# Kernel tuning notes

Measured on AMD Instinct MI355X. Metric: run time of the kernel, lower is better.

## Reference

```python
import jax, jax.numpy as jnp
import numpy as np

N_NODES = 50000
N_EDGES = 600000
IN_FEATS = 128
HIDDEN = 256
OUT_FEATS = 64


def setup_inputs() -> dict:
    key = jax.random.key(0)
    ks = jax.random.split(key, 12)
    inv = lambda n: 1.0 / np.sqrt(n)
    return {
        "x": jax.random.normal(ks[0], (N_NODES, IN_FEATS), dtype=jnp.float32),
        "edge_index": jax.random.randint(ks[1], (2, N_EDGES), 0, N_NODES, dtype=jnp.int64),
        "W_sage": jax.random.normal(ks[2], (IN_FEATS, IN_FEATS), dtype=jnp.float32) * inv(IN_FEATS),
        "W1a": jax.random.normal(ks[3], (IN_FEATS, HIDDEN), dtype=jnp.float32) * inv(IN_FEATS),
        "b1a": jax.random.normal(ks[4], (HIDDEN,), dtype=jnp.float32) * 0.01,
        "W1b": jax.random.normal(ks[5], (HIDDEN, OUT_FEATS), dtype=jnp.float32) * inv(HIDDEN),
        "b1b": jax.random.normal(ks[6], (OUT_FEATS,), dtype=jnp.float32) * 0.01,
        "W2a": jax.random.normal(ks[7], (IN_FEATS, HIDDEN), dtype=jnp.float32) * inv(IN_FEATS),
        "b2a": jax.random.normal(ks[8], (HIDDEN,), dtype=jnp.float32) * 0.01,
        "W2b": jax.random.normal(ks[9], (HIDDEN, OUT_FEATS), dtype=jnp.float32) * inv(HIDDEN),
        "b2b": jax.random.normal(ks[10], (OUT_FEATS,), dtype=jnp.float32) * 0.01,
    }


def reference(x, edge_index, W_sage, W1a, b1a, W1b, b1b, W2a, b2a, W2b, b2b):
    n = x.shape[0]
    src, dst = edge_index[0], edge_index[1]
    # SAGEConv mean aggregation: mean over incoming neighbor (source) features at each target node
    summed = jax.ops.segment_sum(x[src], dst, num_segments=n)          # [N, in]
    deg = jax.ops.segment_sum(jnp.ones_like(src, dtype=x.dtype), dst, num_segments=n)
    mean = summed / jnp.maximum(deg, 1.0)[:, None]                     # nodes w/o neighbors -> 0
    x_1hop = mean @ W_sage                                             # lin_l, no root, no bias
    # dual MLP branches (dropout is identity in eval mode)
    out1 = jax.nn.relu(x @ W1a + b1a) @ W1b + b1b
    out2 = jax.nn.relu(x_1hop @ W2a + b2a) @ W2b + b2b
    return out1 + out2
```

## Files before the change

### kernel.cpp

```cpp
#include <hip/hip_runtime.h>

#define N_NODES 50000
#define N_PAD   50048
#define N_EDGES 600000
#define IN_F 128
#define HID 256
#define OUT_F 64
#define ROWS 16
#define SLOTS 56
#define NBLK (N_PAD / ROWS)
#define EPT 4

typedef __attribute__((ext_vector_type(8))) short bf16x8;
typedef __attribute__((ext_vector_type(4))) float f32x4;

__device__ inline short f2bf(float f) {
    unsigned u = __builtin_bit_cast(unsigned, f);
    u += 0x7fffu + ((u >> 16) & 1u);
    return (short)(u >> 16);
}
__device__ inline float bflo(unsigned u) { return __builtin_bit_cast(float, u << 16); }
__device__ inline float bfhi(unsigned u) { return __builtin_bit_cast(float, u & 0xffff0000u); }

__global__ __launch_bounds__(256) void build_kernel(
    const int* __restrict__ ei, int* __restrict__ cursor,
    unsigned short* __restrict__ esrc)
{
    int t0 = blockIdx.x * (256 * EPT) + threadIdx.x;
    int src[EPT], dst[EPT], p[EPT];
    bool v[EPT];
    #pragma unroll
    for (int i = 0; i < EPT; ++i) {
        int e = t0 + i * 256;
        v[i] = e < N_EDGES;
        int ee = v[i] ? e : 0;
        src[i] = ei[ee];
        dst[i] = ei[N_EDGES + ee];
    }
    #pragma unroll
    for (int i = 0; i < EPT; ++i)
        p[i] = v[i] ? atomicAdd(&cursor[dst[i]], 1) : SLOTS;
    #pragma unroll
    for (int i = 0; i < EPT; ++i)
        if (v[i] && p[i] < SLOTS)
            esrc[(size_t)dst[i] * SLOTS + p[i]] = (unsigned short)src[i];
}

__global__ __launch_bounds__(256) void prep_kernel(
    const float* __restrict__ x, short* __restrict__ xb,
    const float* __restrict__ Wsg, const float* __restrict__ W2a,
    const float* __restrict__ W1a, const float* __restrict__ W1b,
    const float* __restrict__ W2b,
    short* __restrict__ F1a, short* __restrict__ F1b,
    short* __restrict__ Fc,  short* __restrict__ F2b)
{
    const int bid = blockIdx.x, t = threadIdx.x;
    if (bid < 3125) {
        int i = bid * 256 + t;
        float4 a0 = *reinterpret_cast<const float4*>(x + (size_t)i * 8);
        float4 a1 = *reinterpret_cast<const float4*>(x + (size_t)i * 8 + 4);
        bf16x8 v;
        v[0] = f2bf(a0.x); v[1] = f2bf(a0.y); v[2] = f2bf(a0.z); v[3] = f2bf(a0.w);
        v[4] = f2bf(a1.x); v[5] = f2bf(a1.y); v[6] = f2bf(a1.z); v[7] = f2bf(a1.w);
        *reinterpret_cast<bf16x8*>(xb + (size_t)i * 8) = v;
        return;
    }
    int cid = (bid - 3125) * 256 + t;
    if (cid >= 6144 && cid < 10240) {
        int c = cid - 6144;
        int lane = c & 63, rem = c >> 6;
        int ks = rem & 3, nt = rem >> 2;
        int col = nt * 16 + (lane & 15);
        int k0 = ks * 32 + (lane >> 4) * 8;
        float acc[8] = {0.f, 0.f, 0.f, 0.f, 0.f, 0.f, 0.f, 0.f};
        for (int m0 = 0; m0 < 128; m0 += 8) {
            float wcol[8];
            #pragma unroll
            for (int mm = 0; mm < 8; ++mm)
                wcol[mm] = W2a[(size_t)(m0 + mm) * HID + col];
            #pragma unroll
            for (int j = 0; j < 8; ++j) {
                #pragma unroll
                for (int mm = 0; mm < 8; ++mm)
                    acc[j] = fmaf(Wsg[(size_t)(k0 + j) * IN_F + m0 + mm], wcol[mm], acc[j]);
            }
        }
        bf16x8 v;
        #pragma unroll
        for (int j = 0; j < 8; ++j) v[j] = f2bf(acc[j]);
        *reinterpret_cast<bf16x8*>(Fc + (size_t)c * 8) = v;
    } else {
        const float* src; short* dst; int N, KST, base;
        if      (cid < 4096)  { src = W1a; dst = F1a; N = 256; KST = 4; base = 0; }
        else if (cid < 6144)  { src = W1b; dst = F1b; N = 64;  KST = 8; base = 4096; }
        else                  { src = W2b; dst = F2b; N = 64;  KST = 8; base = 10240; }
        int c = cid - base;
        int lane = c & 63;
        int rem = c >> 6;
        int ks = rem % KST;
        int nt = rem / KST;
        int col = nt * 16 + (lane & 15);
        int k0 = ks * 32 + (lane >> 4) * 8;
        bf16x8 v;
        #pragma unroll
        for (int j = 0; j < 8; ++j)
            v[j] = f2bf(src[(size_t)(k0 + j) * N + col]);
        *reinterpret_cast<bf16x8*>(dst + (size_t)c * 8) = v;
    }
}

__device__ inline bf16x8 afrag_lds128(const short* S, int lane, int ks) {
    int row = lane & 15, g = lane >> 4;
    int chunk = (ks * 4 + g) ^ row;
    return *reinterpret_cast<const bf16x8*>(
        reinterpret_cast<const char*>(S) + row * 256 + chunk * 16);
}
__device__ inline bf16x8 afrag_lds256(const short* S, int lane, int ks) {
    int row = lane & 15, g = lane >> 4;
    int chunk = (ks * 4 + g) ^ row;
    return *reinterpret_cast<const bf16x8*>(
        reinterpret_cast<const char*>(S) + row * 512 + chunk * 16);
}

__device__ inline void stage1_relu(const bf16x8 afr[4], short* Hs,
                                   const short* __restrict__ Waf,
                                   const float* __restrict__ ba,
                                   int w, int lane)
{
    const int row16 = lane & 15, g = lane >> 4;
    #pragma unroll
    for (int i = 0; i < 4; ++i) {
        int nt = w * 4 + i;
        f32x4 acc = {0.f, 0.f, 0.f, 0.f};
        __builtin_amdgcn_s_setprio(1);
        #pragma unroll
        for (int ks = 0; ks < 4; ++ks) {
            bf16x8 b = *reinterpret_cast<const bf16x8*>(
                Waf + ((size_t)(nt * 4 + ks) * 64 + lane) * 8);
            acc = __builtin_amdgcn_mfma_f32_16x16x32_bf16(afr[ks], b, acc, 0, 0, 0);
        }
        __builtin_amdgcn_s_setprio(0);
        int col = nt * 16 + row16;
        float bias = ba[col];
        #pragma unroll
        for (int reg = 0; reg < 4; ++reg) {
            int hrow = g * 4 + reg;
            float v = fmaxf(acc[reg] + bias, 0.0f);
            *reinterpret_cast<short*>(reinterpret_cast<char*>(Hs)
                + hrow * 512 + ((((col >> 3) ^ hrow) & 31) * 16) + (col & 7) * 2) = f2bf(v);
        }
    }
}

__device__ inline f32x4 stage2_acc(const short* Hs, const short* __restrict__ Wbf,
                                   int w, int lane, f32x4 acc)
{
    __builtin_amdgcn_s_setprio(1);
    #pragma unroll
    for (int ks = 0; ks < 8; ++ks) {
        bf16x8 a = afrag_lds256(Hs, lane, ks);
        bf16x8 b = *reinterpret_cast<const bf16x8*>(
            Wbf + ((size_t)(w * 8 + ks) * 64 + lane) * 8);
        acc = __builtin_amdgcn_mfma_f32_16x16x32_bf16(a, b, acc, 0, 0, 0);
    }
    __builtin_amdgcn_s_setprio(0);
    return acc;
}

__global__ __launch_bounds__(256) void fused_kernel(
    const short* __restrict__ xb, const unsigned short* __restrict__ esrc,
    const int* __restrict__ deg,
    const short* __restrict__ F1a, const float* __restrict__ b1a,
    const short* __restrict__ F1b, const float* __restrict__ b1b,
    const short* __restrict__ Fc,  const float* __restrict__ b2a,
    const short* __restrict__ F2b, const float* __restrict__ b2b,
    float* __restrict__ out)
{
    __shared__ short Ms[16 * 128];
    __shared__ short Hs[16 * 256];
    const int t = threadIdx.x, w = t >> 6, lane = t & 63;
    const long r0 = (long)blockIdx.x * ROWS;
    const int row16 = lane & 15, g = lane >> 4;

    #pragma unroll
    for (int nn = 0; nn < 4; ++nn) {
        int row = w * 4 + nn;
        long node = r0 + row;
        int d = deg[node]; d = min(d, SLOTS);
        int slot = min(lane, SLOTS - 1);
        int my = esrc[(size_t)node * SLOTS + slot];
        float ax = 0.f, ay = 0.f;
        for (int j = 0; j < d; j += 16) {
            unsigned u[16];
            #pragma unroll
            for (int k = 0; k < 16; ++k) {
                int cidx = min(j + k, d - 1);
                int s = __builtin_amdgcn_readlane(my, cidx);
                u[k] = *reinterpret_cast<const unsigned*>(xb + (size_t)s * IN_F + lane * 2);
            }
            #pragma unroll
            for (int k = 0; k < 16; ++k) {
                float wk = (j + k < d) ? 1.0f : 0.0f;
                ax = fmaf(bflo(u[k]), wk, ax);
                ay = fmaf(bfhi(u[k]), wk, ay);
            }
        }
        float inv = (d > 0) ? 1.0f / (float)d : 0.0f;
        ax *= inv; ay *= inv;
        int chunk = (lane >> 2) ^ row;
        unsigned packed = (unsigned)(unsigned short)f2bf(ax)
                        | ((unsigned)(unsigned short)f2bf(ay) << 16);
        *reinterpret_cast<unsigned*>(reinterpret_cast<char*>(Ms)
            + row * 256 + chunk * 16 + (lane & 3) * 4) = packed;
    }
    __syncthreads();

    {
        bf16x8 afr[4];
        #pragma unroll
        for (int ks = 0; ks < 4; ++ks) afr[ks] = afrag_lds128(Ms, lane, ks);
        stage1_relu(afr, Hs, Fc, b2a, w, lane);
    }
    __syncthreads();

    f32x4 oacc = {0.f, 0.f, 0.f, 0.f};
    oacc = stage2_acc(Hs, F2b, w, lane, oacc);
    __syncthreads();

    {
        bf16x8 afr[4];
        const short* xrow = xb + (size_t)(r0 + row16) * IN_F + g * 8;
        #pragma unroll
        for (int ks = 0; ks < 4; ++ks)
            afr[ks] = *reinterpret_cast<const bf16x8*>(xrow + ks * 32);
        stage1_relu(afr, Hs, F1a, b1a, w, lane);
    }
    __syncthreads();

    oacc = stage2_acc(Hs, F1b, w, lane, oacc);
    {
        int col = w * 16 + row16;
        float bias = b1b[col] + b2b[col];
        #pragma unroll
        for (int reg = 0; reg < 4; ++reg) {
            long row = r0 + g * 4 + reg;
            if (row < N_NODES)
                out[row * OUT_F + col] = oacc[reg] + bias;
        }
    }
}

extern "C" void kernel_launch(void* const* d_in, const int* in_sizes, int n_in,
                              void* d_out, int out_size, void* d_ws, size_t ws_size,
                              hipStream_t stream)
{
    const float* x   = (const float*)d_in[0];
    const int*   ei  = (const int*)d_in[1];
    const float* Wsg = (const float*)d_in[2];
    const float* W1a = (const float*)d_in[3];
    const float* b1a = (const float*)d_in[4];
    const float* W1b = (const float*)d_in[5];
    const float* b1b = (const float*)d_in[6];
    const float* W2a = (const float*)d_in[7];
    const float* b2a = (const float*)d_in[8];
    const float* W2b = (const float*)d_in[9];
    const float* b2b = (const float*)d_in[10];
    float* out = (float*)d_out;

    int* cursor = (int*)d_ws;
    unsigned short* esrc = (unsigned short*)(cursor + N_PAD);
    short* F1a = (short*)(esrc + (size_t)N_PAD * SLOTS);
    short* F1b = F1a + 4096 * 8;
    short* Fc  = F1b + 2048 * 8;
    short* F2b = Fc + 4096 * 8;
    short* xb  = F2b + 2048 * 8;

    hipMemsetAsync(cursor, 0, N_PAD * sizeof(int), stream);
    build_kernel<<<(N_EDGES + 256 * EPT - 1) / (256 * EPT), 256, 0, stream>>>(
        ei, cursor, esrc);
    prep_kernel<<<3173, 256, 0, stream>>>(x, xb, Wsg, W2a, W1a, W1b, W2b,
                                          F1a, F1b, Fc, F2b);
    fused_kernel<<<NBLK, 256, 0, stream>>>(xb, esrc, cursor,
                                           F1a, b1a, F1b, b1b,
                                           Fc, b2a, F2b, b2b, out);
}
```

Baseline: 122.0 us.

## Merge memset into prep, interleave dual MLP branches, pad gather with zero row

Drops the separate hipMemsetAsync and zeroes the cursor inside the prep kernel, which also writes a zero row after xb. Build now runs after prep with one edge per thread. In the fused kernel, the gather uses a wave-uniform degree and sends out-of-range slots to the zero row, so the masked FMAs become plain adds. The two MLP branches are computed together with separate LDS buffers, which removes two barriers and interleaves independent MFMA chains. The cost is more shared memory per block and extra register pressure.

```diff
diff --git a/kernel.cpp b/kernel.cpp
--- a/kernel.cpp
+++ b/kernel.cpp
@@ -9,7 +9,7 @@
 #define ROWS 16
 #define SLOTS 56
 #define NBLK (N_PAD / ROWS)
-#define EPT 4
+#define ZERO_ROW N_NODES
 
 typedef __attribute__((ext_vector_type(8))) short bf16x8;
 typedef __attribute__((ext_vector_type(4))) float f32x4;
@@ -21,30 +21,6 @@
 }
 __device__ inline float bflo(unsigned u) { return __builtin_bit_cast(float, u << 16); }
 __device__ inline float bfhi(unsigned u) { return __builtin_bit_cast(float, u & 0xffff0000u); }
-
-__global__ __launch_bounds__(256) void build_kernel(
-    const int* __restrict__ ei, int* __restrict__ cursor,
-    unsigned short* __restrict__ esrc)
-{
-    int t0 = blockIdx.x * (256 * EPT) + threadIdx.x;
-    int src[EPT], dst[EPT], p[EPT];
-    bool v[EPT];
-    #pragma unroll
-    for (int i = 0; i < EPT; ++i) {
-        int e = t0 + i * 256;
-        v[i] = e < N_EDGES;
-        int ee = v[i] ? e : 0;
-        src[i] = ei[ee];
-        dst[i] = ei[N_EDGES + ee];
-    }
-    #pragma unroll
-    for (int i = 0; i < EPT; ++i)
-        p[i] = v[i] ? atomicAdd(&cursor[dst[i]], 1) : SLOTS;
-    #pragma unroll
-    for (int i = 0; i < EPT; ++i)
-        if (v[i] && p[i] < SLOTS)
-            esrc[(size_t)dst[i] * SLOTS + p[i]] = (unsigned short)src[i];
-}
 
 __global__ __launch_bounds__(256) void prep_kernel(
     const float* __restrict__ x, short* __restrict__ xb,
@@ -52,7 +28,8 @@
     const float* __restrict__ W1a, const float* __restrict__ W1b,
     const float* __restrict__ W2b,
     short* __restrict__ F1a, short* __restrict__ F1b,
-    short* __restrict__ Fc,  short* __restrict__ F2b)
+    short* __restrict__ Fc,  short* __restrict__ F2b,
+    int* __restrict__ cursor)
 {
     const int bid = blockIdx.x, t = threadIdx.x;
     if (bid < 3125) {
@@ -63,6 +40,17 @@
         v[0] = f2bf(a0.x); v[1] = f2bf(a0.y); v[2] = f2bf(a0.z); v[3] = f2bf(a0.w);
         v[4] = f2bf(a1.x); v[5] = f2bf(a1.y); v[6] = f2bf(a1.z); v[7] = f2bf(a1.w);
         *reinterpret_cast<bf16x8*>(xb + (size_t)i * 8) = v;
+        return;
+    }
+    if (bid >= 3200) {
+        int i = (bid - 3200) * 256 + t;
+        bf16x8 z = {0, 0, 0, 0, 0, 0, 0, 0};
+        *reinterpret_cast<bf16x8*>(xb + (size_t)N_NODES * IN_F + (size_t)i * 8) = z;
+        return;
+    }
+    if (bid >= 3173) {
+        for (int i = (bid - 3173) * 256 + t; i < N_PAD; i += 27 * 256)
+            cursor[i] = 0;
         return;
     }
     int cid = (bid - 3125) * 256 + t;
@@ -109,6 +97,18 @@
     }
 }
 
+__global__ __launch_bounds__(256) void build_kernel(
+    const int* __restrict__ ei, int* __restrict__ cursor,
+    unsigned short* __restrict__ esrc)
+{
+    int e = blockIdx.x * 256 + threadIdx.x;
+    if (e >= N_EDGES) return;
+    int src = ei[e];
+    int dst = ei[N_EDGES + e];
+    int p = atomicAdd(&cursor[dst], 1);
+    if (p < SLOTS) esrc[(size_t)dst * SLOTS + p] = (unsigned short)src;
+}
+
 __device__ inline bf16x8 afrag_lds128(const short* S, int lane, int ks) {
     int row = lane & 15, g = lane >> 4;
     int chunk = (ks * 4 + g) ^ row;
@@ -120,51 +120,6 @@
     int chunk = (ks * 4 + g) ^ row;
     return *reinterpret_cast<const bf16x8*>(
         reinterpret_cast<const char*>(S) + row * 512 + chunk * 16);
-}
-
-__device__ inline void stage1_relu(const bf16x8 afr[4], short* Hs,
-                                   const short* __restrict__ Waf,
-                                   const float* __restrict__ ba,
-                                   int w, int lane)
-{
-    const int row16 = lane & 15, g = lane >> 4;
-    #pragma unroll
-    for (int i = 0; i < 4; ++i) {
-        int nt = w * 4 + i;
-        f32x4 acc = {0.f, 0.f, 0.f, 0.f};
-        __builtin_amdgcn_s_setprio(1);
-        #pragma unroll
-        for (int ks = 0; ks < 4; ++ks) {
-            bf16x8 b = *reinterpret_cast<const bf16x8*>(
-                Waf + ((size_t)(nt * 4 + ks) * 64 + lane) * 8);
-            acc = __builtin_amdgcn_mfma_f32_16x16x32_bf16(afr[ks], b, acc, 0, 0, 0);
-        }
-        __builtin_amdgcn_s_setprio(0);
-        int col = nt * 16 + row16;
-        float bias = ba[col];
-        #pragma unroll
-        for (int reg = 0; reg < 4; ++reg) {
-            int hrow = g * 4 + reg;
-            float v = fmaxf(acc[reg] + bias, 0.0f);
-            *reinterpret_cast<short*>(reinterpret_cast<char*>(Hs)
-                + hrow * 512 + ((((col >> 3) ^ hrow) & 31) * 16) + (col & 7) * 2) = f2bf(v);
-        }
-    }
-}
-
-__device__ inline f32x4 stage2_acc(const short* Hs, const short* __restrict__ Wbf,
-                                   int w, int lane, f32x4 acc)
-{
-    __builtin_amdgcn_s_setprio(1);
-    #pragma unroll
-    for (int ks = 0; ks < 8; ++ks) {
-        bf16x8 a = afrag_lds256(Hs, lane, ks);
-        bf16x8 b = *reinterpret_cast<const bf16x8*>(
-            Wbf + ((size_t)(w * 8 + ks) * 64 + lane) * 8);
-        acc = __builtin_amdgcn_mfma_f32_16x16x32_bf16(a, b, acc, 0, 0, 0);
-    }
-    __builtin_amdgcn_s_setprio(0);
-    return acc;
 }
 
 __global__ __launch_bounds__(256) void fused_kernel(
@@ -177,7 +132,8 @@
     float* __restrict__ out)
 {
     __shared__ short Ms[16 * 128];
-    __shared__ short Hs[16 * 256];
+    __shared__ short Hs1[16 * 256];
+    __shared__ short Hs2[16 * 256];
     const int t = threadIdx.x, w = t >> 6, lane = t & 63;
     const long r0 = (long)blockIdx.x * ROWS;
     const int row16 = lane & 15, g = lane >> 4;
@@ -186,26 +142,28 @@
     for (int nn = 0; nn < 4; ++nn) {
         int row = w * 4 + nn;
         long node = r0 + row;
-        int d = deg[node]; d = min(d, SLOTS);
+        int d = min(deg[node], SLOTS);
+        int du = __builtin_amdgcn_readfirstlane(d);
         int slot = min(lane, SLOTS - 1);
         int my = esrc[(size_t)node * SLOTS + slot];
         float ax = 0.f, ay = 0.f;
-        for (int j = 0; j < d; j += 16) {
+        for (int j = 0; j < du; j += 16) {
             unsigned u[16];
             #pragma unroll
             for (int k = 0; k < 16; ++k) {
-                int cidx = min(j + k, d - 1);
-                int s = __builtin_amdgcn_readlane(my, cidx);
-                u[k] = *reinterpret_cast<const unsigned*>(xb + (size_t)s * IN_F + lane * 2);
+                int idx = j + k;
+                int s = (idx < du) ? __builtin_amdgcn_readlane(my, idx)
+                                   : ZERO_ROW;
+                u[k] = *reinterpret_cast<const unsigned*>(
+                    xb + (size_t)s * IN_F + lane * 2);
             }
             #pragma unroll
             for (int k = 0; k < 16; ++k) {
-                float wk = (j + k < d) ? 1.0f : 0.0f;
-                ax = fmaf(bflo(u[k]), wk, ax);
-                ay = fmaf(bfhi(u[k]), wk, ay);
+                ax += bflo(u[k]);
+                ay += bfhi(u[k]);
             }
         }
-        float inv = (d > 0) ? 1.0f / (float)d : 0.0f;
+        float inv = (du > 0) ? 1.0f / (float)du : 0.0f;
         ax *= inv; ay *= inv;
         int chunk = (lane >> 2) ^ row;
         unsigned packed = (unsigned)(unsigned short)f2bf(ax)
@@ -213,31 +171,64 @@
         *reinterpret_cast<unsigned*>(reinterpret_cast<char*>(Ms)
             + row * 256 + chunk * 16 + (lane & 3) * 4) = packed;
     }
+
+    bf16x8 afrA[4];
+    {
+        const short* xrow = xb + (size_t)(r0 + row16) * IN_F + g * 8;
+        #pragma unroll
+        for (int ks = 0; ks < 4; ++ks)
+            afrA[ks] = *reinterpret_cast<const bf16x8*>(xrow + ks * 32);
+    }
     __syncthreads();
 
-    {
-        bf16x8 afr[4];
-        #pragma unroll
-        for (int ks = 0; ks < 4; ++ks) afr[ks] = afrag_lds128(Ms, lane, ks);
-        stage1_relu(afr, Hs, Fc, b2a, w, lane);
+    bf16x8 afrB[4];
+    #pragma unroll
+    for (int ks = 0; ks < 4; ++ks) afrB[ks] = afrag_lds128(Ms, lane, ks);
+    #pragma unroll
+    for (int i = 0; i < 4; ++i) {
+        int nt = w * 4 + i;
+        bf16x8 bA[4], bB[4];
+        #pragma unroll
+        for (int ks = 0; ks < 4; ++ks) {
+            bA[ks] = *reinterpret_cast<const bf16x8*>(
+                F1a + ((size_t)(nt * 4 + ks) * 64 + lane) * 8);
+            bB[ks] = *reinterpret_cast<const bf16x8*>(
+                Fc + ((size_t)(nt * 4 + ks) * 64 + lane) * 8);
+        }
+        f32x4 acc1 = {0.f, 0.f, 0.f, 0.f};
+        f32x4 acc2 = {0.f, 0.f, 0.f, 0.f};
+        #pragma unroll
+        for (int ks = 0; ks < 4; ++ks) {
+            acc1 = __builtin_amdgcn_mfma_f32_16x16x32_bf16(afrA[ks], bA[ks], acc1, 0, 0, 0);
+            acc2 = __builtin_amdgcn_mfma_f32_16x16x32_bf16(afrB[ks], bB[ks], acc2, 0, 0, 0);
+        }
+        int col = nt * 16 + row16;
+        float bias1 = b1a[col], bias2 = b2a[col];
+        #pragma unroll
+        for (int reg = 0; reg < 4; ++reg) {
+            int hrow = g * 4 + reg;
+            int off = hrow * 512 + ((((col >> 3) ^ hrow) & 31) * 16) + (col & 7) * 2;
+            *reinterpret_cast<short*>(reinterpret_cast<char*>(Hs1) + off)
+                = f2bf(fmaxf(acc1[reg] + bias1, 0.0f));
+            *reinterpret_cast<short*>(reinterpret_cast<char*>(Hs2) + off)
+                = f2bf(fmaxf(acc2[reg] + bias2, 0.0f));
+        }
     }
     __syncthreads();
 
-    f32x4 oacc = {0.f, 0.f, 0.f, 0.f};
-    oacc = stage2_acc(Hs, F2b, w, lane, oacc);
-    __syncthreads();
-
-    {
-        bf16x8 afr[4];
-        const short* xrow = xb + (size_t)(r0 + row16) * IN_F + g * 8;
-        #pragma unroll
-        for (int ks = 0; ks < 4; ++ks)
-            afr[ks] = *reinterpret_cast<const bf16x8*>(xrow + ks * 32);
-        stage1_relu(afr, Hs, F1a, b1a, w, lane);
-    }
-    __syncthreads();
-
-    oacc = stage2_acc(Hs, F1b, w, lane, oacc);
+    f32x4 o1 = {0.f, 0.f, 0.f, 0.f};
+    f32x4 o2 = {0.f, 0.f, 0.f, 0.f};
+    #pragma unroll
+    for (int ks = 0; ks < 8; ++ks) {
+        bf16x8 a1 = afrag_lds256(Hs1, lane, ks);
+        bf16x8 b1 = *reinterpret_cast<const bf16x8*>(
+            F1b + ((size_t)(w * 8 + ks) * 64 + lane) * 8);
+        o1 = __builtin_amdgcn_mfma_f32_16x16x32_bf16(a1, b1, o1, 0, 0, 0);
+        bf16x8 a2 = afrag_lds256(Hs2, lane, ks);
+        bf16x8 b2 = *reinterpret_cast<const bf16x8*>(
+            F2b + ((size_t)(w * 8 + ks) * 64 + lane) * 8);
+        o2 = __builtin_amdgcn_mfma_f32_16x16x32_bf16(a2, b2, o2, 0, 0, 0);
+    }
     {
         int col = w * 16 + row16;
         float bias = b1b[col] + b2b[col];
@@ -245,7 +236,7 @@
         for (int reg = 0; reg < 4; ++reg) {
             long row = r0 + g * 4 + reg;
             if (row < N_NODES)
-                out[row * OUT_F + col] = oacc[reg] + bias;
+                out[row * OUT_F + col] = o1[reg] + o2[reg] + bias;
         }
     }
 }
@@ -275,11 +266,9 @@
     short* F2b = Fc + 4096 * 8;
     short* xb  = F2b + 2048 * 8;
 
-    hipMemsetAsync(cursor, 0, N_PAD * sizeof(int), stream);
-    build_kernel<<<(N_EDGES + 256 * EPT - 1) / (256 * EPT), 256, 0, stream>>>(
-        ei, cursor, esrc);
-    prep_kernel<<<3173, 256, 0, stream>>>(x, xb, Wsg, W2a, W1a, W1b, W2b,
-                                          F1a, F1b, Fc, F2b);
+    prep_kernel<<<3203, 256, 0, stream>>>(x, xb, Wsg, W2a, W1a, W1b, W2b,
+                                          F1a, F1b, Fc, F2b, cursor);
+    build_kernel<<<(N_EDGES + 255) / 256, 256, 0, stream>>>(ei, cursor, esrc);
     fused_kernel<<<NBLK, 256, 0, stream>>>(xb, esrc, cursor,
                                            F1a, b1a, F1b, b1b,
                                            Fc, b2a, F2b, b2b, out);
```

Result: faster. 108.1 us (-11.4%).
